# Kernel tuning notes

Measured on AMD Instinct MI355X. Metric: run time of the kernel, lower is better.

## Reference

```python
import jax, jax.numpy as jnp
import numpy as np

N, n, d = 4, 2048, 1024


def setup_inputs() -> dict:
    key = jax.random.key(0)
    k1, k2, k3, k4 = jax.random.split(key, 4)
    x = jax.random.normal(k1, (N, n, d), dtype=jnp.float32)
    mask = jax.random.randint(k2, (N, n, n), 0, 2, dtype=jnp.int32)
    Wqk = jax.random.normal(k3, (d, d), dtype=jnp.float32) * (d ** -0.5)
    Wvc = jax.random.normal(k4, (d, d), dtype=jnp.float32) * (d ** -0.5)
    return {"x": x, "mask": mask, "Wqk": Wqk, "Wvc": Wvc}


def reference(x, mask, Wqk, Wvc):
    # q = Wqk(x): torch Linear computes x @ W^T
    q = jnp.einsum('bnd,ed->bne', x, Wqk)          # [N, n, d]
    scale = jnp.asarray(x.shape[-1], x.dtype) ** 0.5
    scores = jnp.einsum('bnd,bmd->bnm', q, x) / scale  # [N, n, n]
    scores = jnp.where(mask == 0, jnp.asarray(-1e20, scores.dtype), scores)
    attention = jax.nn.softmax(scores, axis=-1)
    attended = jnp.einsum('bnm,bmd->bnd', attention, x)
    return jnp.einsum('bnd,ed->bne', attended, Wvc)
```

## Files before the change

### kernel.cpp

```cpp
#include <hip/hip_runtime.h>
#include <hip/hip_bf16.h>

typedef short bf16x8 __attribute__((ext_vector_type(8)));
typedef short s16x4  __attribute__((ext_vector_type(4)));
typedef short s16x8  __attribute__((ext_vector_type(8)));
typedef float f32x4  __attribute__((ext_vector_type(4)));

static __device__ __forceinline__ void async_cp16(const void* g, void* l) {
  __builtin_amdgcn_global_load_lds(
      (const __attribute__((address_space(1))) unsigned int*)g,
      (__attribute__((address_space(3))) unsigned int*)l, 16, 0, 0);
}

static __device__ __forceinline__ unsigned short f2bf_bits(float f) {
  union { __hip_bfloat16 b; unsigned short u; } cv;
  cv.b = __float2bfloat16(f);
  return cv.u;
}
static __device__ __forceinline__ float bf2f(short u) {
  union { float f; unsigned v; } cv;
  cv.v = ((unsigned)(unsigned short)u) << 16;
  return cv.f;
}

#define BAR() __builtin_amdgcn_s_barrier()
#define VMW(n) do { asm volatile("s_waitcnt vmcnt(" #n ")" ::: "memory"); __builtin_amdgcn_sched_barrier(0); } while (0)

__global__ __launch_bounds__(256) void cvt_all(const float* __restrict__ x,
                                               const float* __restrict__ wqk,
                                               const float* __restrict__ wvc,
                                               __hip_bfloat16* __restrict__ xb,
                                               __hip_bfloat16* __restrict__ wqkb,
                                               __hip_bfloat16* __restrict__ wvcb) {
  const int b = blockIdx.x;
  const float* in;
  __hip_bfloat16* out;
  long base;
  if (b < 8192)       { in = x;   out = xb;   base = (long)b * 1024; }
  else if (b < 9216)  { in = wqk; out = wqkb; base = (long)(b - 8192) * 1024; }
  else                { in = wvc; out = wvcb; base = (long)(b - 9216) * 1024; }
  const long i = base + threadIdx.x * 4;
  const float4 v = *(const float4*)(in + i);
  s16x4 o;
  o[0] = (short)f2bf_bits(v.x);
  o[1] = (short)f2bf_bits(v.y);
  o[2] = (short)f2bf_bits(v.z);
  o[3] = (short)f2bf_bits(v.w);
  *(s16x4*)(out + i) = o;
}

struct GemmDesc {
  const __hip_bfloat16* A; const __hip_bfloat16* B; void* C;
  int lda, ldb, ldc, nT, tpb; long sA, sB, sC; float cscale;
};

template<int MODE, int WM, int WN, int MR_, int MINW>
__global__ __launch_bounds__(512, MINW) void gemm8w(GemmDesc g0, GemmDesc g1, int nb0, int K) {
  constexpr int BM    = WM * MR_ * 16;
  constexpr int BN    = WN * 64;
  constexpr int BOFF  = BM * 64;
  constexpr int BUFSZ = (BM + BN) * 64;
  constexpr int KW    = (BM + BN) / 128;
  __shared__ char lds[3 * BUFSZ];

  const int bid = blockIdx.x, nwg = gridDim.x;
  const int wg = (bid & 7) * (nwg >> 3) + (bid >> 3);
  GemmDesc g = (wg < nb0) ? g0 : g1;
  const int id = (wg < nb0) ? wg : wg - nb0;
  const int bz = id / g.tpb, tl = id - bz * g.tpb;
  const int bm = tl / g.nT, bn = tl - bm * g.nT;
  const long m0 = (long)bm * BM, n0 = (long)bn * BN;
  const __hip_bfloat16* Ab = g.A + bz * g.sA;
  const __hip_bfloat16* Bb = g.B + bz * g.sB;

  const int t = threadIdx.x;
  const int lane = t & 63, w = t >> 6;
  const int wm = w / WN, wn = w % WN;
  const int lr = lane & 15, cs = lane >> 4;

  const int rA  = t >> 2;
  const int dsl = t & 3;
  const int ssl = dsl ^ ((rA >> 1) & 3);
  const __hip_bfloat16* aSt0 = Ab + (m0 + rA) * g.lda + ssl * 8;
  const __hip_bfloat16* aSt1 = Ab + (m0 + 128 + rA) * g.lda + ssl * 8;
  const __hip_bfloat16* bSt0 = Bb + (n0 + rA) * g.ldb + ssl * 8;
  const __hip_bfloat16* bSt1 = Bb + (n0 + 128 + rA) * g.ldb + ssl * 8;

  const int axor = ((lr >> 1) & 3) << 4;
  int aRd[MR_], bRd[4];
  #pragma unroll
  for (int mm = 0; mm < MR_; ++mm)
    aRd[mm] = (wm * (MR_ * 16) + mm * 16 + lr) * 64 + ((cs << 4) ^ axor);
  #pragma unroll
  for (int nf = 0; nf < 4; ++nf)
    bRd[nf] = BOFF + (wn * 64 + nf * 16 + lr) * 64 + ((cs << 4) ^ axor);

  f32x4 acc[MR_][4] = {};

  #define STAGE(kt, base) do { \
    async_cp16(aSt0 + (long)(kt) * 32, lds + (base) + t * 16); \
    async_cp16(aSt1 + (long)(kt) * 32, lds + (base) + 8192 + t * 16); \
    async_cp16(bSt0 + (long)(kt) * 32, lds + (base) + BOFF + t * 16); \
    if constexpr (BN == 256) \
      async_cp16(bSt1 + (long)(kt) * 32, lds + (base) + BOFF + 8192 + t * 16); \
  } while (0)
  #define VM_KW() do { if constexpr (KW == 4) { VMW(4); } else { VMW(3); } } while (0)

  const int nt = K >> 5;
  STAGE(0, 0);
  STAGE(1, BUFSZ);
  VM_KW();
  BAR();

  int rb = 0, sb = 2 * BUFSZ;
  for (int tt = 0; tt < nt; ++tt) {
    bf16x8 af[MR_], bq[4];
    #pragma unroll
    for (int mm = 0; mm < MR_; ++mm)
      af[mm] = *(const bf16x8*)(lds + rb + aRd[mm]);
    #pragma unroll
    for (int nf = 0; nf < 4; ++nf)
      bq[nf] = *(const bf16x8*)(lds + rb + bRd[nf]);
    if (tt + 2 < nt) STAGE(tt + 2, sb);
    #pragma unroll
    for (int mm = 0; mm < MR_; ++mm)
      #pragma unroll
      for (int nf = 0; nf < 4; ++nf)
        acc[mm][nf] = __builtin_amdgcn_mfma_f32_16x16x32_bf16(af[mm], bq[nf], acc[mm][nf], 0, 0, 0);
    if (tt + 2 < nt) { VM_KW(); } else { VMW(0); }
    BAR();
    rb = (rb == 2 * BUFSZ) ? 0 : rb + BUFSZ;
    sb = (sb == 2 * BUFSZ) ? 0 : sb + BUFSZ;
  }
  #undef STAGE
  #undef VM_KW

  const long crow0 = m0 + wm * (MR_ * 16) + cs * 4;
  const long ccol0 = n0 + wn * 64 + lr;
  if (MODE == 0) {
    float* C = (float*)g.C + bz * g.sC;
    #pragma unroll
    for (int mm = 0; mm < MR_; ++mm)
      #pragma unroll
      for (int nf = 0; nf < 4; ++nf)
        #pragma unroll
        for (int rr = 0; rr < 4; ++rr)
          C[(crow0 + mm * 16 + rr) * g.ldc + ccol0 + nf * 16] = acc[mm][nf][rr];
  } else {
    __hip_bfloat16* C = (__hip_bfloat16*)g.C + bz * g.sC;
    #pragma unroll
    for (int mm = 0; mm < MR_; ++mm)
      #pragma unroll
      for (int nf = 0; nf < 4; ++nf)
        #pragma unroll
        for (int rr = 0; rr < 4; ++rr)
          C[(crow0 + mm * 16 + rr) * g.ldc + ccol0 + nf * 16] =
              __float2bfloat16(acc[mm][nf][rr] * g.cscale);
  }
}

__global__ __launch_bounds__(256) void softmax_rows(__hip_bfloat16* __restrict__ S,
                                                    const int* __restrict__ Mask) {
  const long row = blockIdx.x;
  short* srow = (short*)(S + row * 2048);
  const int* mrow = Mask + row * 2048;
  const int t = threadIdx.x;
  const s16x8 sv = *(const s16x8*)(srow + t * 8);
  const int4 q0 = *(const int4*)(mrow + t * 8);
  const int4 q1 = *(const int4*)(mrow + t * 8 + 4);
  float f[8];
  f[0] = q0.x ? bf2f(sv[0]) : -1e20f;
  f[1] = q0.y ? bf2f(sv[1]) : -1e20f;
  f[2] = q0.z ? bf2f(sv[2]) : -1e20f;
  f[3] = q0.w ? bf2f(sv[3]) : -1e20f;
  f[4] = q1.x ? bf2f(sv[4]) : -1e20f;
  f[5] = q1.y ? bf2f(sv[5]) : -1e20f;
  f[6] = q1.z ? bf2f(sv[6]) : -1e20f;
  f[7] = q1.w ? bf2f(sv[7]) : -1e20f;

  float mx = f[0];
  #pragma unroll
  for (int i = 1; i < 8; ++i) mx = fmaxf(mx, f[i]);
  #pragma unroll
  for (int off = 32; off > 0; off >>= 1) mx = fmaxf(mx, __shfl_xor(mx, off));
  __shared__ float redm[4], reds[4];
  if ((t & 63) == 0) redm[t >> 6] = mx;
  __syncthreads();
  mx = fmaxf(fmaxf(redm[0], redm[1]), fmaxf(redm[2], redm[3]));

  float e[8];
  float s = 0.f;
  #pragma unroll
  for (int i = 0; i < 8; ++i) { e[i] = __expf(f[i] - mx); s += e[i]; }
  #pragma unroll
  for (int off = 32; off > 0; off >>= 1) s += __shfl_xor(s, off);
  if ((t & 63) == 0) reds[t >> 6] = s;
  __syncthreads();
  s = reds[0] + reds[1] + reds[2] + reds[3];
  const float inv = 1.f / s;

  s16x8 o;
  #pragma unroll
  for (int i = 0; i < 8; ++i) o[i] = (short)f2bf_bits(e[i] * inv);
  *(s16x8*)(srow + t * 8) = o;
}

extern "C" void kernel_launch(void* const* d_in, const int* in_sizes, int n_in,
                              void* d_out, int out_size, void* d_ws, size_t ws_size,
                              hipStream_t stream) {
  const float* x   = (const float*)d_in[0];
  const int*   msk = (const int*)d_in[1];
  const float* Wqk = (const float*)d_in[2];
  const float* Wvc = (const float*)d_in[3];
  float* out = (float*)d_out;
  char* ws = (char*)d_ws;

  __hip_bfloat16* xb   = (__hip_bfloat16*)(ws + 0);
  __hip_bfloat16* qb   = (__hip_bfloat16*)(ws + 16777216);
  __hip_bfloat16* vT   = (__hip_bfloat16*)(ws + 33554432);
  __hip_bfloat16* wqkb = (__hip_bfloat16*)(ws + 50331648);
  __hip_bfloat16* wvcb = (__hip_bfloat16*)(ws + 52428800);
  __hip_bfloat16* Sbf  = (__hip_bfloat16*)(ws + 54525952);

  cvt_all<<<dim3(10240), 256, 0, stream>>>(x, Wqk, Wvc, xb, wqkb, wvcb);

  GemmDesc gq{xb,   wqkb, qb, 1024, 1024, 1024, 4, 128, 0L, 0L, 0L, 0.03125f};
  GemmDesc gv{wvcb, xb,   vT, 1024, 1024, 2048, 8, 32, 0L, 2097152L, 2097152L, 1.f};
  gemm8w<1, 2, 4, 8, 2><<<dim3(256), 512, 0, stream>>>(gq, gv, 128, 1024);

  GemmDesc gs{qb, xb, Sbf, 1024, 1024, 2048, 8, 64, 2097152L, 2097152L, 4194304L, 1.f};
  gemm8w<1, 2, 4, 8, 2><<<dim3(256), 512, 0, stream>>>(gs, gs, 256, 1024);

  softmax_rows<<<dim3(8192), 256, 0, stream>>>(Sbf, msk);

  GemmDesc go{Sbf, vT, out, 2048, 2048, 1024, 8, 64, 4194304L, 2097152L, 2097152L, 1.f};
  gemm8w<0, 4, 2, 4, 4><<<dim3(256), 512, 0, stream>>>(go, go, 256, 2048);
}
```

Baseline: 145.2 us.

## Add 256x256 ping-pong GEMM kernel with staggered staging for QK and scores

Adds a new bf16 MFMA GEMM kernel that uses a 256x256 tile, 128 KB of LDS split into two buffers, and a hand-scheduled sequence of half-tile async loads interleaved with MFMA blocks, barriers and s_setprio. It replaces the generic gemm8w kernel for the Q/V projection and the score GEMM. The aim is to overlap global-to-LDS transfers with matrix math more finely and to raise arithmetic intensity per tile. The cost is a large LDS footprint and many registers (8x4 accumulators), which limits occupancy. The manual wait counts and barriers are fragile if K or the tile counts change.

After: 142.9 us. Within noise of the previous version (-1.6%).

```diff
diff --git a/kernel.cpp b/kernel.cpp
--- a/kernel.cpp
+++ b/kernel.cpp
@@ -24,7 +24,9 @@
 }
 
 #define BAR() __builtin_amdgcn_s_barrier()
-#define VMW(n) do { asm volatile("s_waitcnt vmcnt(" #n ")" ::: "memory"); __builtin_amdgcn_sched_barrier(0); } while (0)
+#define SBZ() __builtin_amdgcn_sched_barrier(0)
+#define LGKM0() do { asm volatile("s_waitcnt lgkmcnt(0)" ::: "memory"); SBZ(); } while (0)
+#define VMW(n) do { asm volatile("s_waitcnt vmcnt(" #n ")" ::: "memory"); SBZ(); } while (0)
 
 __global__ __launch_bounds__(256) void cvt_all(const float* __restrict__ x,
                                                const float* __restrict__ wqk,
@@ -54,6 +56,142 @@
   int lda, ldb, ldc, nT, tpb; long sA, sB, sC; float cscale;
 };
 
+template<int MODE>
+__global__ __launch_bounds__(512, 2) void gemm8p(GemmDesc g0, GemmDesc g1, int nb0, int K) {
+  __shared__ char lds[131072];
+  const int bid = blockIdx.x, nwg = gridDim.x;
+  const int wg = (bid & 7) * (nwg >> 3) + (bid >> 3);
+  GemmDesc g = (wg < nb0) ? g0 : g1;
+  const int id = (wg < nb0) ? wg : wg - nb0;
+  const int bz = id / g.tpb, tl = id - bz * g.tpb;
+  const int bm = tl / g.nT, bn = tl - bm * g.nT;
+  const long m0 = (long)bm * 256, n0 = (long)bn * 256;
+  const __hip_bfloat16* Ab = g.A + bz * g.sA;
+  const __hip_bfloat16* Bb = g.B + bz * g.sB;
+
+  const int t = threadIdx.x, lane = t & 63, w = t >> 6;
+  const int wm = w >> 2, wn = w & 3;
+  const int lr = lane & 15, cs = lane >> 4;
+
+  const int srow = t >> 3;
+  const int sslot = (t & 7) ^ (srow & 7);
+  const __hip_bfloat16* aP[2][2];
+  const __hip_bfloat16* bP[2][2];
+  #pragma unroll
+  for (int h = 0; h < 2; ++h)
+    #pragma unroll
+    for (int i = 0; i < 2; ++i) {
+      aP[h][i] = Ab + (m0 + h * 128 + i * 64 + srow) * g.lda + sslot * 8;
+      bP[h][i] = Bb + (n0 + h * 128 + i * 64 + srow) * g.ldb + sslot * 8;
+    }
+
+  int aOf[8], bOf[4];
+  #pragma unroll
+  for (int mm = 0; mm < 8; ++mm)
+    aOf[mm] = wm * 16384 + (mm * 16 + lr) * 128 + ((cs ^ (lr & 7)) << 4);
+  #pragma unroll
+  for (int nf = 0; nf < 4; ++nf)
+    bOf[nf] = 32768 + (wn >> 1) * 16384 + ((wn & 1) * 64 + nf * 16 + lr) * 128 +
+              ((cs ^ (lr & 7)) << 4);
+  f32x4 acc[8][4] = {};
+  bf16x8 af[4][2], bqA[2][2], bqB[2][2];
+
+  #define STG(P, h, kt, dbase) do { \
+    async_cp16(P[h][0] + (long)(kt) * 64, lds + (dbase) + t * 16); \
+    async_cp16(P[h][1] + (long)(kt) * 64, lds + (dbase) + 8192 + t * 16); } while (0)
+  #define RD_AF(mb, bufb) do { _Pragma("unroll") for (int mm_ = 0; mm_ < 4; ++mm_) { \
+      af[mm_][0] = *(const bf16x8*)(lds + (bufb) + aOf[(mb) * 4 + mm_]); \
+      af[mm_][1] = *(const bf16x8*)(lds + (bufb) + (aOf[(mb) * 4 + mm_] ^ 64)); } } while (0)
+  #define RD_BQ(dst, nb, bufb) do { _Pragma("unroll") for (int nf_ = 0; nf_ < 2; ++nf_) { \
+      dst[nf_][0] = *(const bf16x8*)(lds + (bufb) + bOf[(nb) * 2 + nf_]); \
+      dst[nf_][1] = *(const bf16x8*)(lds + (bufb) + (bOf[(nb) * 2 + nf_] ^ 64)); } } while (0)
+  #define MM16(BQ, NB, MB) do { \
+    __builtin_amdgcn_s_setprio(1); \
+    _Pragma("unroll") for (int ks_ = 0; ks_ < 2; ++ks_) \
+      _Pragma("unroll") for (int mm_ = 0; mm_ < 4; ++mm_) \
+        _Pragma("unroll") for (int nf_ = 0; nf_ < 2; ++nf_) \
+          acc[(MB) + mm_][(NB) + nf_] = __builtin_amdgcn_mfma_f32_16x16x32_bf16( \
+              af[mm_][ks_], BQ[nf_][ks_], acc[(MB) + mm_][(NB) + nf_], 0, 0, 0); \
+    __builtin_amdgcn_s_setprio(0); } while (0)
+
+  const int nt = K >> 6, nJ = nt >> 1;
+  STG(bP, 0, 0, 32768); STG(bP, 1, 0, 49152);
+  STG(aP, 0, 0, 0);     STG(aP, 1, 0, 16384);
+  STG(bP, 0, 1, 65536 + 32768); STG(bP, 1, 1, 65536 + 49152);
+  VMW(4);
+  BAR(); SBZ();
+
+  for (int j = 0; j < nJ; ++j) {
+    const bool full = (j + 1 < nJ);
+    const int tb = 2 * j + 1, ta2 = 2 * j + 2, tb2 = 2 * j + 3;
+    RD_AF(0, 0); RD_BQ(bqA, 0, 0);
+    STG(aP, 0, tb, 65536);
+    LGKM0();
+    MM16(bqA, 0, 0);
+    BAR(); SBZ();
+    RD_BQ(bqB, 1, 0);
+    STG(aP, 1, tb, 65536 + 16384);
+    LGKM0();
+    MM16(bqB, 2, 0);
+    BAR(); SBZ();
+    RD_AF(1, 0);
+    if (full) STG(bP, 0, ta2, 32768);
+    LGKM0();
+    MM16(bqB, 2, 4);
+    BAR(); SBZ();
+    if (full) STG(bP, 1, ta2, 49152);
+    MM16(bqA, 0, 4);
+    if (full) { VMW(4); } else { VMW(0); }
+    BAR(); SBZ();
+    RD_AF(0, 65536); RD_BQ(bqA, 0, 65536);
+    if (full) STG(aP, 0, ta2, 0);
+    LGKM0();
+    MM16(bqA, 0, 0);
+    BAR(); SBZ();
+    RD_BQ(bqB, 1, 65536);
+    if (full) STG(aP, 1, ta2, 16384);
+    LGKM0();
+    MM16(bqB, 2, 0);
+    BAR(); SBZ();
+    RD_AF(1, 65536);
+    if (full) STG(bP, 0, tb2, 65536 + 32768);
+    LGKM0();
+    MM16(bqB, 2, 4);
+    BAR(); SBZ();
+    if (full) STG(bP, 1, tb2, 65536 + 49152);
+    MM16(bqA, 0, 4);
+    if (full) { VMW(4); } else { VMW(0); }
+    BAR(); SBZ();
+  }
+  #undef STG
+  #undef RD_AF
+  #undef RD_BQ
+  #undef MM16
+
+  const long crow0 = m0 + wm * 128 + cs * 4;
+  const long ccol0 = n0 + wn * 64 + lr;
+  if (MODE == 0) {
+    float* C = (float*)g.C + bz * g.sC;
+    #pragma unroll
+    for (int mm = 0; mm < 8; ++mm)
+      #pragma unroll
+      for (int nf = 0; nf < 4; ++nf)
+        #pragma unroll
+        for (int rr = 0; rr < 4; ++rr)
+          C[(crow0 + mm * 16 + rr) * g.ldc + ccol0 + nf * 16] = acc[mm][nf][rr];
+  } else {
+    __hip_bfloat16* C = (__hip_bfloat16*)g.C + bz * g.sC;
+    #pragma unroll
+    for (int mm = 0; mm < 8; ++mm)
+      #pragma unroll
+      for (int nf = 0; nf < 4; ++nf)
+        #pragma unroll
+        for (int rr = 0; rr < 4; ++rr)
+          C[(crow0 + mm * 16 + rr) * g.ldc + ccol0 + nf * 16] =
+              __float2bfloat16(acc[mm][nf][rr] * g.cscale);
+  }
+}
+
 template<int MODE, int WM, int WN, int MR_, int MINW>
 __global__ __launch_bounds__(512, MINW) void gemm8w(GemmDesc g0, GemmDesc g1, int nb0, int K) {
   constexpr int BM    = WM * MR_ * 16;
@@ -226,10 +364,10 @@
 
   GemmDesc gq{xb,   wqkb, qb, 1024, 1024, 1024, 4, 128, 0L, 0L, 0L, 0.03125f};
   GemmDesc gv{wvcb, xb,   vT, 1024, 1024, 2048, 8, 32, 0L, 2097152L, 2097152L, 1.f};
-  gemm8w<1, 2, 4, 8, 2><<<dim3(256), 512, 0, stream>>>(gq, gv, 128, 1024);
+  gemm8p<1><<<dim3(256), 512, 0, stream>>>(gq, gv, 128, 1024);
 
   GemmDesc gs{qb, xb, Sbf, 1024, 1024, 2048, 8, 64, 2097152L, 2097152L, 4194304L, 1.f};
-  gemm8w<1, 2, 4, 8, 2><<<dim3(256), 512, 0, stream>>>(gs, gs, 256, 1024);
+  gemm8p<1><<<dim3(256), 512, 0, stream>>>(gs, gs, 256, 1024);
 
   softmax_rows<<<dim3(8192), 256, 0, stream>>>(Sbf, msk);
 
```
